# Kernel tuning notes

Measured on AMD Instinct MI355X. Metric: run time of the kernel, lower is better.

The kernel has to match this reference:

```python
import jax, jax.numpy as jnp
import numpy as np

D_MODEL = 1472
N_HEADS = 6
D_KV = 64
INNER = N_HEADS * D_KV
NUM_BUCKETS = 32
MAX_DIST = 128


def _relative_position_bucket(relative_position, bidirectional=True,
                              num_buckets=NUM_BUCKETS, max_distance=MAX_DIST):
    ret = jnp.zeros_like(relative_position)
    if bidirectional:
        num_buckets //= 2
        ret = ret + (relative_position > 0).astype(jnp.int32) * num_buckets
        rel = jnp.abs(relative_position)
    else:
        rel = -jnp.minimum(relative_position, 0)
    max_exact = num_buckets // 2
    is_small = rel < max_exact
    rel_f = jnp.maximum(rel, 1).astype(jnp.float32)
    large = max_exact + (
        jnp.log(rel_f / max_exact) / np.log(max_distance / max_exact)
        * (num_buckets - max_exact)
    ).astype(jnp.int32)
    large = jnp.minimum(large, num_buckets - 1)
    return ret + jnp.where(is_small, rel, large)


def _position_bias(q_len, k_len, rel_bias):
    # rel_bias: [num_buckets, n_heads]
    ctx = jnp.arange(q_len)[:, None]
    mem = jnp.arange(k_len)[None, :]
    buckets = _relative_position_bucket(mem - ctx, bidirectional=True)
    values = rel_bias[buckets]                 # [Q, K, H]
    return jnp.transpose(values, (2, 0, 1))[None]  # [1, H, Q, K]


def setup_inputs() -> dict:
    key = jax.random.key(0)
    ks = jax.random.split(key, 8)
    B, S = 4, 2048
    scale = 0.02
    return {
        "kv_sequences": jax.random.normal(ks[0], (B, S, D_MODEL), jnp.float32),
        "q_sequences": jax.random.normal(ks[1], (B, S, D_MODEL), jnp.float32),
        "mask": jnp.zeros((B, 1, S, S), jnp.float32),
        "WQ": jax.random.normal(ks[2], (D_MODEL, INNER), jnp.float32) * scale,
        "WK": jax.random.normal(ks[3], (D_MODEL, INNER), jnp.float32) * scale,
        "WV": jax.random.normal(ks[4], (D_MODEL, INNER), jnp.float32) * scale,
        "WO": jax.random.normal(ks[5], (INNER, D_MODEL), jnp.float32) * scale,
        "rel_bias": jax.random.normal(ks[6], (NUM_BUCKETS, N_HEADS), jnp.float32) * scale,
    }


def reference(kv_sequences, q_sequences, mask, WQ, WK, WV, WO, rel_bias):
    B, Kl, _ = kv_sequences.shape
    Ql = q_sequences.shape[1]
    # projections -> [B, H, L, d_kv]
    q = (q_sequences @ WQ).reshape(B, Ql, N_HEADS, D_KV).transpose(0, 2, 1, 3)
    k = (kv_sequences @ WK).reshape(B, Kl, N_HEADS, D_KV).transpose(0, 2, 1, 3)
    v = (kv_sequences @ WV).reshape(B, Kl, N_HEADS, D_KV).transpose(0, 2, 1, 3)
    # T5-style: no 1/sqrt(d) scaling
    logits = jnp.einsum("bhqd,bhkd->bhqk", q, k)
    logits = logits + _position_bias(Ql, Kl, rel_bias)
    logits = logits + mask
    attn = jax.nn.softmax(logits.astype(jnp.float32), axis=-1).astype(logits.dtype)
    out = jnp.einsum("bhqk,bhkd->bhqd", attn, v)
    out = out.transpose(0, 2, 1, 3).reshape(B, Ql, INNER)
    return out @ WO
```

## Files before the change

kernel.cpp:

```cpp
#include <hip/hip_runtime.h>
#include <hip/hip_fp16.h>
#include <cstdint>

#define DM    1472
#define NH    6
#define DKV   64
#define INNER 384
#define BATCH 4
#define SEQ   2048
#define LOG2E 1.4426950408889634f

typedef __attribute__((ext_vector_type(8))) _Float16 half8;
typedef __attribute__((ext_vector_type(4))) _Float16 half4;
typedef __attribute__((ext_vector_type(4))) float f32x4;

__device__ __forceinline__ void gload16(const void* g, const void* l) {
  __builtin_amdgcn_global_load_lds((const __attribute__((address_space(1))) void*)g,
                                   (__attribute__((address_space(3))) void*)l, 16, 0, 0);
}

__global__ void prep_weights(const float* __restrict__ WQ, const float* __restrict__ WK,
                             const float* __restrict__ WV, const float* __restrict__ WO,
                             _Float16* __restrict__ WqT, _Float16* __restrict__ WkT,
                             _Float16* __restrict__ WvT, _Float16* __restrict__ WoT) {
  int idx = blockIdx.x * blockDim.x + threadIdx.x;
  const int per = DM * INNER;
  if (idx >= 4 * per) return;
  int which = idx / per;
  int i = idx - which * per;
  if (which < 3) {
    const float* W = which == 0 ? WQ : (which == 1 ? WK : WV);
    _Float16* T = which == 0 ? WqT : (which == 1 ? WkT : WvT);
    int k = i / INNER, n = i - (i / INNER) * INNER;
    T[(size_t)n * DM + k] = (_Float16)W[i];
  } else {
    int k = i / DM, n = i - (i / DM) * DM;
    WoT[(size_t)n * INNER + k] = (_Float16)WO[i];
  }
}

__global__ void prep_bias(const float* __restrict__ rel_bias, float* __restrict__ biasS) {
  int idx = blockIdx.x * blockDim.x + threadIdx.x;
  const int TOT = NH * 4 * 4104;
  if (idx >= TOT) return;
  int h = idx / (4 * 4104);
  int rem = idx - h * 4 * 4104;
  int cc = rem / 4104;
  int i = rem - cc * 4104;
  int j = i + cc; if (j > 4094) j = 4094;
  int d = j - 2047;
  int ret = d > 0 ? 16 : 0;
  int a = d < 0 ? -d : d;
  int bucket;
  if (a < 8) bucket = ret + a;
  else {
    int large;
    if      (a >= 91) large = 15;
    else if (a >= 64) large = 14;
    else if (a >= 46) large = 13;
    else if (a >= 32) large = 12;
    else if (a >= 23) large = 11;
    else if (a >= 16) large = 10;
    else if (a >= 12) large = 9;
    else              large = 8;
    bucket = ret + large;
  }
  biasS[idx] = rel_bias[bucket * NH + h] * LOG2E;
}

__global__ __launch_bounds__(256) void prep_maskflags(const float* __restrict__ mask,
                                                      int* __restrict__ flags) {
  const int bid = blockIdx.x;
  const int kh = bid & 1;
  const int qt = (bid >> 1) & 31;
  const int b = bid >> 6;
  const int tid = threadIdx.x;
  __shared__ int fl[16];
  if (tid < 16) fl[tid] = 0;
  __syncthreads();
  const float* base = mask + ((size_t)(b * SEQ + qt * 64)) * SEQ + kh * 1024 + tid * 4;
  bool nz = false;
  for (int q = 0; q < 64; ++q) {
    f32x4 v = *(const f32x4*)(base + (size_t)q * SEQ);
    nz |= (v[0] != 0.f) | (v[1] != 0.f) | (v[2] != 0.f) | (v[3] != 0.f);
  }
  if (nz) fl[tid >> 4] = 1;
  __syncthreads();
  if (tid < 16) flags[(size_t)b * 1024 + qt * 32 + kh * 16 + tid] = fl[tid];
}

__global__ __launch_bounds__(256) void proj_gemm(
    const float* __restrict__ Xq, const float* __restrict__ Xkv,
    const _Float16* __restrict__ WqT, const _Float16* __restrict__ WkvT,
    _Float16* __restrict__ Qo, _Float16* __restrict__ Ko, _Float16* __restrict__ Vto) {
  const int bm = blockIdx.x, by = blockIdx.y;
  const bool isQ = by < 3;
  const float* __restrict__ X = isQ ? Xq : Xkv;
  const _Float16* __restrict__ WT = isQ ? (WqT + (size_t)by * 128 * DM)
                                        : (WkvT + (size_t)(by - 3) * 128 * DM);

  __shared__ alignas(16) float    As[2][128 * 32];
  __shared__ alignas(16) _Float16 Bs[2][128 * 32];

  const int tid = threadIdx.x;
  const int lane = tid & 63, wave = tid >> 6;
  const int wm = wave >> 1, wn = wave & 1;
  const int l15 = lane & 15, lg = lane >> 4;

  f32x4 acc[4][4] = {};

  const int aoff = 4 * ((lane & 7) ^ (lane >> 3));
  const float* asrc[4];
#pragma unroll
  for (int c = 0; c < 4; ++c)
    asrc[c] = X + (size_t)(bm * 128 + (wave * 4 + c) * 8 + (lane >> 3)) * DM + aoff;
  const int boff = 8 * ((lane & 3) ^ ((lane >> 3) & 3));
  const _Float16* bsrc[2];
#pragma unroll
  for (int c = 0; c < 2; ++c)
    bsrc[c] = WT + (size_t)((wave * 2 + c) * 16 + (lane >> 2)) * DM + boff;

  const int NT = DM / 32;

#pragma unroll
  for (int c = 0; c < 4; ++c)
    gload16(asrc[c], (const char*)&As[0][0] + (wave * 4 + c) * 1024);
#pragma unroll
  for (int c = 0; c < 2; ++c)
    gload16(bsrc[c], (const char*)&Bs[0][0] + (wave * 2 + c) * 1024);
  __syncthreads();

  for (int t = 0; t < NT; ++t) {
    if (t + 1 < NT) {
      const int nb = (t + 1) & 1;
      const int kf = (t + 1) * 32;
#pragma unroll
      for (int c = 0; c < 4; ++c)
        gload16(asrc[c] + kf, (const char*)&As[nb][0] + (wave * 4 + c) * 1024);
#pragma unroll
      for (int c = 0; c < 2; ++c)
        gload16(bsrc[c] + kf, (const char*)&Bs[nb][0] + (wave * 2 + c) * 1024);
    }

    const char* Ab = (const char*)&As[t & 1][0];
    const char* Bb = (const char*)&Bs[t & 1][0];
    half8 af[4], bf[4];
#pragma unroll
    for (int m = 0; m < 4; ++m) {
      int r = wm * 64 + m * 16 + l15;
      int s = (r & 7) << 4;
      f32x4 x0 = *(const f32x4*)(Ab + r * 128 + ((lg * 32) ^ s));
      f32x4 x1 = *(const f32x4*)(Ab + r * 128 + ((lg * 32 + 16) ^ s));
      half8 h;
#pragma unroll
      for (int j = 0; j < 4; ++j) { h[j] = (_Float16)x0[j]; h[4 + j] = (_Float16)x1[j]; }
      af[m] = h;
    }
#pragma unroll
    for (int n = 0; n < 4; ++n) {
      int r = wn * 64 + n * 16 + l15;
      bf[n] = *(const half8*)(Bb + r * 64 + ((lg * 16) ^ (((r >> 1) & 3) << 4)));
    }

    __builtin_amdgcn_s_setprio(1);
#pragma unroll
    for (int m = 0; m < 4; ++m)
#pragma unroll
      for (int n = 0; n < 4; ++n)
        acc[m][n] = __builtin_amdgcn_mfma_f32_16x16x32_f16(af[m], bf[n], acc[m][n], 0, 0, 0);
    __builtin_amdgcn_s_setprio(0);

    __syncthreads();
  }

#pragma unroll
  for (int m = 0; m < 4; ++m)
#pragma unroll
    for (int n = 0; n < 4; ++n)
#pragma unroll
      for (int r = 0; r < 4; ++r) {
        int gm = bm * 128 + wm * 64 + m * 16 + lg * 4 + r;
        int gnl = wn * 64 + n * 16 + l15;
        int b = gm >> 11, s = gm & 2047;
        float av = acc[m][n][r];
        if (isQ) {
          int gn = by * 128 + gnl;
          int h = gn >> 6, dd = gn & 63;
          Qo[((size_t)(b * NH + h) * SEQ + s) * DKV + dd] = (_Float16)(av * LOG2E);
        } else {
          int gn = (by - 3) * 128 + gnl;
          if (gn < INNER) {
            int h = gn >> 6, dd = gn & 63;
            Ko[((size_t)(b * NH + h) * SEQ + s) * DKV + dd] = (_Float16)av;
          } else {
            int gnv = gn - INNER;
            int h = gnv >> 6, dd = gnv & 63;
            Vto[((size_t)(b * NH + h) * DKV + dd) * SEQ + s] = (_Float16)av;
          }
        }
      }
}

__global__ __launch_bounds__(256, 4) void attn_kernel(
    const _Float16* __restrict__ Q, const _Float16* __restrict__ K, const _Float16* __restrict__ Vt,
    const float* __restrict__ biasS, const float* __restrict__ mask,
    const int* __restrict__ mflags, _Float16* __restrict__ AO) {
  const int bid = blockIdx.x;
  const int g = (bid & 7) * 96 + (bid >> 3);
  const int bh = g >> 5, qb = g & 31;
  const int b = bh / NH, h = bh - b * NH;
  const int q0 = qb * 64;
  const int NT = SEQ / 64;

  const int tid = threadIdx.x, lane = tid & 63, wave = tid >> 6;
  const int l15 = lane & 15, lg = lane >> 4;

  __shared__ alignas(16) _Float16 Ks[2][64 * 64];
  __shared__ alignas(16) _Float16 Vs[2][64 * 64];
  __shared__ alignas(16) _Float16 Ps[4][16 * 64];

  const size_t bhS = (size_t)bh * SEQ;
  const int qq = q0 + wave * 16 + l15;

  const _Float16* Qbase = Q + (bhS + q0 + wave * 16) * DKV;
  half8 qf0 = *(const half8*)(Qbase + (size_t)l15 * DKV + lg * 8);
  half8 qf1 = *(const half8*)(Qbase + (size_t)l15 * DKV + 32 + lg * 8);

  const float* maskrow = mask + (size_t)b * SEQ * SEQ + (size_t)qq * SEQ + lg * 4;
  const int c = (3 - l15) & 3;
  const float* bbase = biasS + (size_t)(h * 4 + c) * 4104 + (lg * 4 - qq + 2047 - c);
  const int* mfl = mflags + b * 1024 + qb * 32;

  float m_r = -1e30f, l_acc = 0.f;
  f32x4 oacc[4] = {};

  const int rl = lane >> 3;
  const int sw = ((lane & 7) ^ rl) * 8;
  const _Float16* Kd0 = K + (bhS + wave * 16 + rl) * DKV + sw;
  const _Float16* Kd1 = Kd0 + 8 * DKV;
  const _Float16* Vd0 = Vt + ((size_t)bh * DKV + wave * 16 + rl) * SEQ + sw;
  const _Float16* Vd1 = Vd0 + 8 * SEQ;
  char* KsB = (char*)&Ks[0][0];
  char* VsB = (char*)&Vs[0][0];
  char* PsB = (char*)&Ps[wave][0];
  const int dmaLds = wave * 2048;

  gload16(Kd0, KsB + dmaLds);
  gload16(Kd1, KsB + dmaLds + 1024);
  gload16(Vd0, VsB + dmaLds);
  gload16(Vd1, VsB + dmaLds + 1024);
  __syncthreads();

  for (int t = 0; t < NT; ++t) {
    const int mflag = mfl[t];
    if (t + 1 < NT) {
      const int nb = (t + 1) & 1;
      gload16(Kd0 + (size_t)(t + 1) * 64 * DKV, KsB + nb * 8192 + dmaLds);
      gload16(Kd1 + (size_t)(t + 1) * 64 * DKV, KsB + nb * 8192 + dmaLds + 1024);
      gload16(Vd0 + (t + 1) * 64, VsB + nb * 8192 + dmaLds);
      gload16(Vd1 + (t + 1) * 64, VsB + nb * 8192 + dmaLds + 1024);
    }
    const char* Kb = KsB + (t & 1) * 8192;
    const char* Vb = VsB + (t & 1) * 8192;

    f32x4 sacc[4] = {};
    __builtin_amdgcn_s_setprio(1);
#pragma unroll
    for (int nf = 0; nf < 4; ++nf) {
      int kr = nf * 16 + l15;
      const char* rb = Kb + kr * 128;
      half8 kf0 = *(const half8*)(rb + ((lg ^ (kr & 7)) << 4));
      half8 kf1 = *(const half8*)(rb + (((4 + lg) ^ (kr & 7)) << 4));
      sacc[nf] = __builtin_amdgcn_mfma_f32_16x16x32_f16(kf0, qf0, sacc[nf], 0, 0, 0);
      sacc[nf] = __builtin_amdgcn_mfma_f32_16x16x32_f16(kf1, qf1, sacc[nf], 0, 0, 0);
    }
    __builtin_amdgcn_s_setprio(0);

    float sv[4][4], fm[4];
#pragma unroll
    for (int nf = 0; nf < 4; ++nf) {
      f32x4 bv = *(const f32x4*)(bbase + t * 64 + nf * 16);
#pragma unroll
      for (int r = 0; r < 4; ++r)
        sv[nf][r] = sacc[nf][r] + bv[r];
    }
    if (mflag) {
#pragma unroll
      for (int nf = 0; nf < 4; ++nf) {
        f32x4 mv = *(const f32x4*)(maskrow + t * 64 + nf * 16);
#pragma unroll
        for (int r = 0; r < 4; ++r)
          sv[nf][r] += mv[r] * LOG2E;
      }
    }
#pragma unroll
    for (int nf = 0; nf < 4; ++nf)
      fm[nf] = fmaxf(fmaxf(sv[nf][0], sv[nf][1]), fmaxf(sv[nf][2], sv[nf][3]));
    float mx = fmaxf(fmaxf(fm[0], fm[1]), fmaxf(fm[2], fm[3]));
    mx = fmaxf(mx, __shfl_xor(mx, 16));
    mx = fmaxf(mx, __shfl_xor(mx, 32));

    if (!__all(mx <= m_r + 8.0f)) {
      float mnew = fmaxf(m_r, mx);
      float sc_ = __builtin_amdgcn_exp2f(m_r - mnew);
      m_r = mnew;
      l_acc *= sc_;
      f32x4 scv;
#pragma unroll
      for (int r = 0; r < 4; ++r) scv[r] = __shfl(sc_, lg * 4 + r);
#pragma unroll
      for (int df = 0; df < 4; ++df) oacc[df] *= scv;
    }

    float rs = 0.f;
#pragma unroll
    for (int nf = 0; nf < 4; ++nf) {
      half4 ph;
#pragma unroll
      for (int r = 0; r < 4; ++r) {
        float p = __builtin_amdgcn_exp2f(sv[nf][r] - m_r);
        rs += p;
        ph[r] = (_Float16)p;
      }
      *(half4*)(PsB + l15 * 128 + ((((nf << 1) + (lg >> 1)) ^ (l15 & 7)) << 4) + ((lg & 1) << 3)) = ph;
    }
    l_acc += rs;

    __builtin_amdgcn_s_setprio(1);
#pragma unroll
    for (int ks = 0; ks < 2; ++ks) {
      half8 pa = *(const half8*)(PsB + l15 * 128 + ((((ks << 2) + lg) ^ (l15 & 7)) << 4));
#pragma unroll
      for (int df = 0; df < 4; ++df) {
        int vr = df * 16 + l15;
        half8 vv = *(const half8*)(Vb + vr * 128 + ((((ks << 2) + lg) ^ (vr & 7)) << 4));
        oacc[df] = __builtin_amdgcn_mfma_f32_16x16x32_f16(pa, vv, oacc[df], 0, 0, 0);
      }
    }
    __builtin_amdgcn_s_setprio(0);

    __syncthreads();
  }

  l_acc += __shfl_xor(l_acc, 16);
  l_acc += __shfl_xor(l_acc, 32);
  f32x4 lv;
#pragma unroll
  for (int r = 0; r < 4; ++r) lv[r] = __shfl(l_acc, lg * 4 + r);
#pragma unroll
  for (int df = 0; df < 4; ++df) {
    int dd = df * 16 + l15;
#pragma unroll
    for (int r = 0; r < 4; ++r) {
      int qrow = q0 + wave * 16 + lg * 4 + r;
      AO[((size_t)(b * SEQ + qrow)) * INNER + h * DKV + dd] = (_Float16)(oacc[df][r] / lv[r]);
    }
  }
}

__global__ __launch_bounds__(256) void out_gemm(
    const _Float16* __restrict__ A, const _Float16* __restrict__ BT, float* __restrict__ C) {
  __shared__ alignas(16) _Float16 As[2][128 * 32];
  __shared__ alignas(16) _Float16 Bs[2][64 * 32];

  const int tid = threadIdx.x, lane = tid & 63, wave = tid >> 6;
  const int wm = wave >> 1, wn = wave & 1;
  const int bm = blockIdx.x, bn = blockIdx.y;
  const int l15 = lane & 15, lg = lane >> 4;

  f32x4 acc[4][2] = {};

  const int rl4 = (lane >> 2) & 3;
  const int soff = ((lane & 3) ^ rl4) * 8;
  const _Float16* ad0 = A + (size_t)(bm * 128 + (wave * 2) * 16 + (lane >> 2)) * INNER + soff;
  const _Float16* ad1 = ad0 + (size_t)16 * INNER;
  const _Float16* bd0 = BT + (size_t)(bn * 64 + wave * 16 + (lane >> 2)) * INNER + soff;
  char* AsB = (char*)&As[0][0];
  char* BsB = (char*)&Bs[0][0];
  const int aLds = wave * 2048;
  const int bLds = wave * 1024;

  const int NT = INNER / 32;

  gload16(ad0, AsB + aLds);
  gload16(ad1, AsB + aLds + 1024);
  gload16(bd0, BsB + bLds);
  __syncthreads();

  for (int t = 0; t < NT; ++t) {
    if (t + 1 < NT) {
      const int nb = (t + 1) & 1;
      const int kf = (t + 1) * 32;
      gload16(ad0 + kf, AsB + nb * 8192 + aLds);
      gload16(ad1 + kf, AsB + nb * 8192 + aLds + 1024);
      gload16(bd0 + kf, BsB + nb * 4096 + bLds);
    }

    const char* Ab = AsB + (t & 1) * 8192;
    const char* Bb = BsB + (t & 1) * 4096;
    half8 af[4], bf[2];
#pragma unroll
    for (int m = 0; m < 4; ++m) {
      int r = wm * 64 + m * 16 + l15;
      af[m] = *(const half8*)(Ab + r * 64 + (((lg ^ (r & 3))) << 4));
    }
#pragma unroll
    for (int n = 0; n < 2; ++n) {
      int r = wn * 32 + n * 16 + l15;
      bf[n] = *(const half8*)(Bb + r * 64 + (((lg ^ (r & 3))) << 4));
    }
    __builtin_amdgcn_s_setprio(1);
#pragma unroll
    for (int m = 0; m < 4; ++m)
#pragma unroll
      for (int n = 0; n < 2; ++n)
        acc[m][n] = __builtin_amdgcn_mfma_f32_16x16x32_f16(af[m], bf[n], acc[m][n], 0, 0, 0);
    __builtin_amdgcn_s_setprio(0);

    __syncthreads();
  }

#pragma unroll
  for (int m = 0; m < 4; ++m)
#pragma unroll
    for (int n = 0; n < 2; ++n)
#pragma unroll
      for (int r = 0; r < 4; ++r) {
        int gm = bm * 128 + wm * 64 + m * 16 + lg * 4 + r;
        int gn = bn * 64 + wn * 32 + n * 16 + l15;
        C[(size_t)gm * DM + gn] = acc[m][n][r];
      }
}

extern "C" void kernel_launch(void* const* d_in, const int* in_sizes, int n_in,
                              void* d_out, int out_size, void* d_ws, size_t ws_size,
                              hipStream_t stream) {
  const float* kv   = (const float*)d_in[0];
  const float* qs   = (const float*)d_in[1];
  const float* mask = (const float*)d_in[2];
  const float* WQ   = (const float*)d_in[3];
  const float* WK   = (const float*)d_in[4];
  const float* WV   = (const float*)d_in[5];
  const float* WO   = (const float*)d_in[6];
  const float* rb   = (const float*)d_in[7];
  float* out = (float*)d_out;
  char* ws = (char*)d_ws;

  const size_t WT_BYTES  = (size_t)INNER * DM * 2;
  const size_t QKV_BYTES = (size_t)BATCH * NH * SEQ * DKV * 2;
  _Float16* WqT = (_Float16*)(ws);
  _Float16* WkT = (_Float16*)(ws + WT_BYTES);
  _Float16* WvT = (_Float16*)(ws + 2 * WT_BYTES);
  _Float16* WoT = (_Float16*)(ws + 3 * WT_BYTES);
  _Float16* Qh  = (_Float16*)(ws + 4 * WT_BYTES);
  _Float16* Kh  = (_Float16*)(ws + 4 * WT_BYTES + QKV_BYTES);
  _Float16* Vth = (_Float16*)(ws + 4 * WT_BYTES + 2 * QKV_BYTES);
  _Float16* AO  = (_Float16*)(ws + 4 * WT_BYTES + 3 * QKV_BYTES);
  float* biasS  = (float*)(ws + 4 * WT_BYTES + 4 * QKV_BYTES);
  int* mflags   = (int*)(ws + 4 * WT_BYTES + 4 * QKV_BYTES + (size_t)NH * 4 * 4104 * 4);

  hipLaunchKernelGGL(prep_weights, dim3((4 * DM * INNER + 255) / 256), dim3(256), 0, stream,
                     WQ, WK, WV, WO, WqT, WkT, WvT, WoT);
  hipLaunchKernelGGL(prep_bias, dim3((NH * 4 * 4104 + 255) / 256), dim3(256), 0, stream, rb, biasS);
  hipLaunchKernelGGL(prep_maskflags, dim3(BATCH * 32 * 2), dim3(256), 0, stream, mask, mflags);
  hipLaunchKernelGGL(proj_gemm, dim3(64, 9), dim3(256), 0, stream,
                     qs, kv, WqT, WkT, Qh, Kh, Vth);
  hipLaunchKernelGGL(attn_kernel, dim3(768), dim3(256), 0, stream,
                     Qh, Kh, Vth, biasS, mask, mflags, AO);
  hipLaunchKernelGGL(out_gemm, dim3(64, 23), dim3(256), 0, stream, AO, WoT, out);
}
```

Baseline: 179.9 us.

## Prefetch two tiles ahead with explicit vmcnt waits in projection and attention loops

Both the projection GEMM and the flash-attention loop now issue global-to-LDS loads two iterations ahead. Each iteration waits with a partial s_waitcnt vmcnt that lets the newest tile's loads stay in flight, instead of a full __syncthreads that drains all outstanding loads. The buffer being refilled is the one just consumed, after a second barrier. This keeps more memory traffic overlapped with MFMA work, at the cost of relying on exact counts of outstanding vector-memory ops, which the compiler's own scheduling could break.

New measurement: 178.1 us. No clear change (-1.0%).

```diff
diff --git a/kernel.cpp b/kernel.cpp
--- a/kernel.cpp
+++ b/kernel.cpp
@@ -128,19 +128,18 @@
 #pragma unroll
   for (int c = 0; c < 2; ++c)
     gload16(bsrc[c], (const char*)&Bs[0][0] + (wave * 2 + c) * 1024);
-  __syncthreads();
+#pragma unroll
+  for (int c = 0; c < 4; ++c)
+    gload16(asrc[c] + 32, (const char*)&As[1][0] + (wave * 4 + c) * 1024);
+#pragma unroll
+  for (int c = 0; c < 2; ++c)
+    gload16(bsrc[c] + 32, (const char*)&Bs[1][0] + (wave * 2 + c) * 1024);
 
   for (int t = 0; t < NT; ++t) {
-    if (t + 1 < NT) {
-      const int nb = (t + 1) & 1;
-      const int kf = (t + 1) * 32;
-#pragma unroll
-      for (int c = 0; c < 4; ++c)
-        gload16(asrc[c] + kf, (const char*)&As[nb][0] + (wave * 4 + c) * 1024);
-#pragma unroll
-      for (int c = 0; c < 2; ++c)
-        gload16(bsrc[c] + kf, (const char*)&Bs[nb][0] + (wave * 2 + c) * 1024);
-    }
+    if (t + 1 < NT) asm volatile("s_waitcnt vmcnt(6)" ::: "memory");
+    else            asm volatile("s_waitcnt vmcnt(0)" ::: "memory");
+    __builtin_amdgcn_s_barrier();
+    __builtin_amdgcn_sched_barrier(0);
 
     const char* Ab = (const char*)&As[t & 1][0];
     const char* Bb = (const char*)&Bs[t & 1][0];
@@ -170,7 +169,17 @@
         acc[m][n] = __builtin_amdgcn_mfma_f32_16x16x32_f16(af[m], bf[n], acc[m][n], 0, 0, 0);
     __builtin_amdgcn_s_setprio(0);
 
-    __syncthreads();
+    __builtin_amdgcn_sched_barrier(0);
+    __builtin_amdgcn_s_barrier();
+    if (t + 2 < NT) {
+      const int kf = (t + 2) * 32;
+#pragma unroll
+      for (int c = 0; c < 4; ++c)
+        gload16(asrc[c] + kf, (const char*)&As[t & 1][0] + (wave * 4 + c) * 1024);
+#pragma unroll
+      for (int c = 0; c < 2; ++c)
+        gload16(bsrc[c] + kf, (const char*)&Bs[t & 1][0] + (wave * 2 + c) * 1024);
+    }
   }
 
 #pragma unroll
@@ -249,17 +258,18 @@
   gload16(Kd1, KsB + dmaLds + 1024);
   gload16(Vd0, VsB + dmaLds);
   gload16(Vd1, VsB + dmaLds + 1024);
-  __syncthreads();
+  gload16(Kd0 + 64 * DKV, KsB + 8192 + dmaLds);
+  gload16(Kd1 + 64 * DKV, KsB + 8192 + dmaLds + 1024);
+  gload16(Vd0 + 64, VsB + 8192 + dmaLds);
+  gload16(Vd1 + 64, VsB + 8192 + dmaLds + 1024);
 
   for (int t = 0; t < NT; ++t) {
+    if (t + 1 < NT) asm volatile("s_waitcnt vmcnt(4)" ::: "memory");
+    else            asm volatile("s_waitcnt vmcnt(0)" ::: "memory");
+    __builtin_amdgcn_s_barrier();
+    __builtin_amdgcn_sched_barrier(0);
+
     const int mflag = mfl[t];
-    if (t + 1 < NT) {
-      const int nb = (t + 1) & 1;
-      gload16(Kd0 + (size_t)(t + 1) * 64 * DKV, KsB + nb * 8192 + dmaLds);
-      gload16(Kd1 + (size_t)(t + 1) * 64 * DKV, KsB + nb * 8192 + dmaLds + 1024);
-      gload16(Vd0 + (t + 1) * 64, VsB + nb * 8192 + dmaLds);
-      gload16(Vd1 + (t + 1) * 64, VsB + nb * 8192 + dmaLds + 1024);
-    }
     const char* Kb = KsB + (t & 1) * 8192;
     const char* Vb = VsB + (t & 1) * 8192;
 
@@ -339,7 +349,16 @@
     }
     __builtin_amdgcn_s_setprio(0);
 
-    __syncthreads();
+    __builtin_amdgcn_sched_barrier(0);
+    __builtin_amdgcn_s_barrier();
+    if (t + 2 < NT) {
+      char* kb = KsB + (t & 1) * 8192 + dmaLds;
+      char* vb_ = VsB + (t & 1) * 8192 + dmaLds;
+      gload16(Kd0 + (size_t)(t + 2) * 64 * DKV, kb);
+      gload16(Kd1 + (size_t)(t + 2) * 64 * DKV, kb + 1024);
+      gload16(Vd0 + (t + 2) * 64, vb_);
+      gload16(Vd1 + (t + 2) * 64, vb_ + 1024);
+    }
   }
 
   l_acc += __shfl_xor(l_acc, 16);
```
